# Optimization experiments

Measured on AMD Instinct MI355X. Metric: run time of the kernel, lower is better.

## Reference

```python
import jax, jax.numpy as jnp
import numpy as np

HEADS = 8
MAX_REL = 256
D_MODEL = 512
FFN_DIM = 2048
LN_EPS = 1e-3  # keras LayerNormalization default
NEG_INF = -1e9


def _layer_norm(x, gamma, beta):
    mu = jnp.mean(x, axis=-1, keepdims=True)
    var = jnp.var(x, axis=-1, keepdims=True)
    return (x - mu) * jax.lax.rsqrt(var + LN_EPS) * gamma + beta


def _mhra(q_in, k_in, v_in, mask, p):
    """Multi-head relative-position (Shaw-style) attention.
    mask: (B, Lq, Lk), 1.0 = masked position (added as -1e9).
    """
    B, Lq, D = q_in.shape
    Lk = k_in.shape[1]
    H = HEADS
    depth = D // H
    q = (q_in @ p['Wq'] + p['bq']).reshape(B, Lq, H, depth).transpose(0, 2, 1, 3)
    k = (k_in @ p['Wk'] + p['bk']).reshape(B, Lk, H, depth).transpose(0, 2, 1, 3)
    v = (v_in @ p['Wv'] + p['bv']).reshape(B, Lk, H, depth).transpose(0, 2, 1, 3)
    # content logits (B,H,Lq,Lk)
    logits = jnp.einsum('bhqd,bhkd->bhqk', q, k)
    # relative-position logits: project q onto clipped relative embeddings
    rel_q = jnp.einsum('bhqd,rd->bhqr', q, p['rel_emb'])  # (B,H,Lq,2K+1)
    rel_idx = jnp.clip(jnp.arange(Lk)[None, :] - jnp.arange(Lq)[:, None],
                       -MAX_REL, MAX_REL) + MAX_REL  # (Lq,Lk)
    rel_logits = jnp.take_along_axis(
        rel_q, jnp.broadcast_to(rel_idx[None, None], (B, H, Lq, Lk)), axis=-1)
    scores = (logits + rel_logits) / jnp.sqrt(jnp.asarray(depth, q.dtype))
    scores = scores + mask[:, None, :, :] * NEG_INF
    weights = jax.nn.softmax(scores, axis=-1)
    out = jnp.einsum('bhqk,bhkd->bhqd', weights, v)
    out = out.transpose(0, 2, 1, 3).reshape(B, Lq, D)
    out = out @ p['Wo'] + p['bo']
    return out, weights


def _make_attn_params(key, prefix):
    ks = jax.random.split(key, 5)
    s = 0.02
    return {
        prefix + 'Wq': jax.random.normal(ks[0], (D_MODEL, D_MODEL), jnp.float32) * s,
        prefix + 'bq': jnp.zeros((D_MODEL,), jnp.float32),
        prefix + 'Wk': jax.random.normal(ks[1], (D_MODEL, D_MODEL), jnp.float32) * s,
        prefix + 'bk': jnp.zeros((D_MODEL,), jnp.float32),
        prefix + 'Wv': jax.random.normal(ks[2], (D_MODEL, D_MODEL), jnp.float32) * s,
        prefix + 'bv': jnp.zeros((D_MODEL,), jnp.float32),
        prefix + 'Wo': jax.random.normal(ks[3], (D_MODEL, D_MODEL), jnp.float32) * s,
        prefix + 'bo': jnp.zeros((D_MODEL,), jnp.float32),
        prefix + 'rel_emb': jax.random.normal(ks[4], (2 * MAX_REL + 1, D_MODEL // HEADS), jnp.float32) * s,
        prefix + 'ln_g': jnp.ones((D_MODEL,), jnp.float32),
        prefix + 'ln_b': jnp.zeros((D_MODEL,), jnp.float32),
    }


def setup_inputs() -> dict:
    key = jax.random.key(0)
    ks = jax.random.split(key, 8)
    B, Lq, Lk = 8, 1024, 1024
    inputs = jax.random.normal(ks[0], (B, Lq, D_MODEL), jnp.float32)
    enc_kv = jax.random.normal(ks[1], (B, Lk, D_MODEL), jnp.float32)
    padding_mask = jnp.zeros((B, Lq, Lk), jnp.float32)  # no encoder padding
    causal = (jnp.arange(Lk)[None, :] > jnp.arange(Lq)[:, None]).astype(jnp.float32)
    lookahead_mask = jnp.broadcast_to(causal[None], (B, Lq, Lq)).astype(jnp.float32)
    d = {'inputs': inputs, 'enc_kv': enc_kv,
         'padding_mask': padding_mask, 'lookahead_mask': lookahead_mask,
         'training': 0}
    d.update(_make_attn_params(ks[2], 'sa_'))
    d.update(_make_attn_params(ks[3], 'ca_'))
    s = 0.02
    d['ffn_W1'] = jax.random.normal(ks[4], (D_MODEL, FFN_DIM), jnp.float32) * s
    d['ffn_b1'] = jnp.zeros((FFN_DIM,), jnp.float32)
    d['ffn_W2'] = jax.random.normal(ks[5], (FFN_DIM, D_MODEL), jnp.float32) * s
    d['ffn_b2'] = jnp.zeros((D_MODEL,), jnp.float32)
    d['ffn_ln_g'] = jnp.ones((D_MODEL,), jnp.float32)
    d['ffn_ln_b'] = jnp.zeros((D_MODEL,), jnp.float32)
    return d


def reference(inputs, enc_kv, padding_mask, lookahead_mask, training,
              sa_Wq, sa_bq, sa_Wk, sa_bk, sa_Wv, sa_bv, sa_Wo, sa_bo,
              sa_rel_emb, sa_ln_g, sa_ln_b,
              ca_Wq, ca_bq, ca_Wk, ca_bk, ca_Wv, ca_bv, ca_Wo, ca_bo,
              ca_rel_emb, ca_ln_g, ca_ln_b,
              ffn_W1, ffn_b1, ffn_W2, ffn_b2, ffn_ln_g, ffn_ln_b):
    sa = {'Wq': sa_Wq, 'bq': sa_bq, 'Wk': sa_Wk, 'bk': sa_bk,
          'Wv': sa_Wv, 'bv': sa_bv, 'Wo': sa_Wo, 'bo': sa_bo,
          'rel_emb': sa_rel_emb}
    ca = {'Wq': ca_Wq, 'bq': ca_bq, 'Wk': ca_Wk, 'bk': ca_bk,
          'Wv': ca_Wv, 'bv': ca_bv, 'Wo': ca_Wo, 'bo': ca_bo,
          'rel_emb': ca_rel_emb}
    # self attention + residual + norm (dropout identity at inference)
    attn_out, attn_w = _mhra(inputs, inputs, inputs, lookahead_mask, sa)
    attn_out = _layer_norm(inputs + attn_out, sa_ln_g, sa_ln_b)
    # cross attention + residual + norm
    ca_out, ca_w = _mhra(attn_out, enc_kv, enc_kv, padding_mask, ca)
    ca_out = _layer_norm(attn_out + ca_out, ca_ln_g, ca_ln_b)
    # pointwise FFN + residual + norm
    h = jax.nn.relu(ca_out @ ffn_W1 + ffn_b1) @ ffn_W2 + ffn_b2
    out = _layer_norm(h + ca_out, ffn_ln_g, ffn_ln_b)
    return out, attn_w, ca_w
```

## Files before the change

kernel.cpp:

```cpp
#include <hip/hip_runtime.h>
#include <hip/hip_bf16.h>
#include <cstdio>


typedef __attribute__((ext_vector_type(8))) short short8v;
typedef __attribute__((ext_vector_type(4))) short short4v;
typedef __attribute__((ext_vector_type(4))) float f32x4;

static __device__ __forceinline__ unsigned short f2bf(float f) {
    unsigned int u = __float_as_uint(f);
    unsigned int r = (u + 0x7fffu + ((u >> 16) & 1u)) >> 16;
    return (unsigned short)r;
}
static __device__ __forceinline__ float bf2f(unsigned short s) {
    return __uint_as_float(((unsigned int)s) << 16);
}

static __device__ __forceinline__ f32x4 mfma_bf16(short8v a, short8v b, f32x4 c) {
    return __builtin_amdgcn_mfma_f32_16x16x32_bf16(a, b, c, 0, 0, 0);
}

static __device__ __forceinline__ void async16(const void* g, void* l) {
    __builtin_amdgcn_global_load_lds(
        (const __attribute__((address_space(1))) unsigned int*)g,
        (__attribute__((address_space(3))) unsigned int*)l,
        16, 0, 0);
}

static __device__ __forceinline__ int swz8(int bid, int nwg) {
    return (bid & 7) * (nwg >> 3) + (bid >> 3);
}


static __device__ __forceinline__ void gemm_core(
    unsigned short* As, unsigned short* Bs,
    const unsigned short* __restrict__ A, int lda,
    const unsigned short* __restrict__ BT, int ldb,
    const float* __restrict__ bias, float* __restrict__ Cf,
    unsigned short* __restrict__ Cb, int ldc,
    int m0, int n0, int Kblk, int relu)
{
    const int t = threadIdx.x, lane = t & 63, w = t >> 6;
    const int wm = w >> 1, wn = w & 1;
    const int g = lane >> 4, l15 = lane & 15;
    f32x4 acc[4][4];
#pragma unroll
    for (int m = 0; m < 4; ++m)
#pragma unroll
        for (int n = 0; n < 4; ++n) acc[m][n] = (f32x4){0.f, 0.f, 0.f, 0.f};

    const int sgl8 = (lane & 7) ^ ((lane >> 3) & 7);
    for (int k0 = 0; k0 < Kblk; k0 += 64) {
#pragma unroll
        for (int i = 0; i < 4; ++i) {
            int rbase = w * 32 + i * 8;
            async16(A  + (size_t)(m0 + rbase + (lane >> 3)) * lda + k0 + sgl8 * 8,
                    As + rbase * 64);
            async16(BT + (size_t)(n0 + rbase + (lane >> 3)) * ldb + k0 + sgl8 * 8,
                    Bs + rbase * 64);
        }
        __syncthreads();
#pragma unroll
        for (int kk = 0; kk < 2; ++kk) {
            short8v a[4], b[4];
#pragma unroll
            for (int m = 0; m < 4; ++m) {
                int row = wm * 64 + m * 16 + l15;
                a[m] = *(const short8v*)&As[row * 64 + (((kk * 4 + g) ^ (row & 7))) * 8];
            }
#pragma unroll
            for (int n = 0; n < 4; ++n) {
                int row = wn * 64 + n * 16 + l15;
                b[n] = *(const short8v*)&Bs[row * 64 + (((kk * 4 + g) ^ (row & 7))) * 8];
            }
#pragma unroll
            for (int m = 0; m < 4; ++m)
#pragma unroll
                for (int n = 0; n < 4; ++n)
                    acc[m][n] = mfma_bf16(a[m], b[n], acc[m][n]);
        }
        __syncthreads();
    }
#pragma unroll
    for (int m = 0; m < 4; ++m) {
        int gm = m0 + wm * 64 + m * 16 + (lane >> 4) * 4;
#pragma unroll
        for (int n = 0; n < 4; ++n) {
            int gn = n0 + wn * 64 + n * 16 + (lane & 15);
            float bv = bias ? bias[gn] : 0.f;
#pragma unroll
            for (int j = 0; j < 4; ++j) {
                float v = acc[m][n][j] + bv;
                if (relu) v = fmaxf(v, 0.f);
                size_t off = (size_t)(gm + j) * ldc + gn;
                if (Cf) Cf[off] = v;
                if (Cb) Cb[off] = f2bf(v);
            }
        }
    }
}

__global__ __launch_bounds__(256) void gemm_std(
    const unsigned short* __restrict__ A, int lda,
    const unsigned short* __restrict__ BT, int ldb,
    const float* __restrict__ bias,
    float* __restrict__ Cf, unsigned short* __restrict__ Cb,
    int N, int Kblk, int relu)
{
    __shared__ __attribute__((aligned(16))) unsigned short As[128 * 64];
    __shared__ __attribute__((aligned(16))) unsigned short Bs[128 * 64];
    const int kz = blockIdx.z;
    const int nwg = gridDim.x * gridDim.y;
    const int s = swz8(blockIdx.x + gridDim.x * blockIdx.y, nwg);
    const int bx = s % gridDim.x, by = s / gridDim.x;
    const size_t part = (size_t)kz * gridDim.y * 128 * N;
    gemm_core(As, Bs, A + kz * Kblk, lda, BT + kz * Kblk, ldb,
              kz == 0 ? bias : nullptr,
              Cf ? Cf + part : nullptr, Cb, N,
              by * 128, bx * 128, Kblk, relu);
}

__global__ __launch_bounds__(256) void gemm_ca(
    const unsigned short* __restrict__ Ekv, const unsigned short* __restrict__ Xq,
    const unsigned short* __restrict__ WkvT, const unsigned short* __restrict__ WqT,
    const float* __restrict__ bkv, const float* __restrict__ bq,
    unsigned short* __restrict__ KV, unsigned short* __restrict__ Q)
{
    __shared__ __attribute__((aligned(16))) unsigned short As[128 * 64];
    __shared__ __attribute__((aligned(16))) unsigned short Bs[128 * 64];
    const int nwg = gridDim.x * gridDim.y;
    const int s = swz8(blockIdx.x + gridDim.x * blockIdx.y, nwg);
    const int bx = s % gridDim.x, by = s / gridDim.x;
    if (bx < 8)
        gemm_core(As, Bs, Ekv, 512, WkvT, 512, bkv, nullptr, KV, 1024,
                  by * 128, bx * 128, 512, 0);
    else
        gemm_core(As, Bs, Xq, 512, WqT, 512, bq, nullptr, Q, 512,
                  by * 128, (bx - 8) * 128, 512, 0);
}

__global__ __launch_bounds__(256, 3) void fused_attn(
    const unsigned short* __restrict__ Qp, int qstride,
    const unsigned short* __restrict__ Kp, int kstride,
    const unsigned short* __restrict__ Vt,
    const unsigned short* __restrict__ relW,
    const unsigned short* __restrict__ maskb,
    float* __restrict__ Wout,
    unsigned short* __restrict__ Hout)
{
    __shared__ __attribute__((aligned(16))) unsigned short Qs[16 * 64];
    __shared__ __attribute__((aligned(16))) unsigned short U[24576];
    __shared__ float Red[2][4][16];
    __shared__ unsigned short R512[16];
    unsigned short* Ks   = U;
    unsigned short* Pl   = U;
    unsigned short* RelV = U + 16384;
    unsigned short* Vs   = U + 16384;
    const int t = threadIdx.x, lane = t & 63, w = t >> 6;
    const int g = lane >> 4, l15 = lane & 15;
    const int s = swz8(blockIdx.x + gridDim.x * blockIdx.y, 4096);
    const int bh = s >> 6, b = bh >> 3, h = bh & 7;
    const int q0 = (s & 63) * 16;
    const int sgl8 = (lane & 7) ^ ((lane >> 3) & 7);

    if (w < 2) {
        int row = w * 8 + (lane >> 3);
        async16(Qp + (size_t)(b * 1024 + q0 + row) * qstride + h * 64 + sgl8 * 8,
                &Qs[w * 512]);
    }
    __syncthreads();

    short8v qa[2];
#pragma unroll
    for (int kk = 0; kk < 2; ++kk)
        qa[kk] = *(const short8v*)&Qs[l15 * 64 + (((kk * 4 + g) ^ (l15 & 7))) * 8];

    auto relTile = [&](int rs) {
        int rc = rs * 16 + l15;
        int re = rc > 512 ? 512 : rc;
        short8v b0 = *(const short8v*)(relW + (size_t)re * 64 + g * 8);
        short8v b1 = *(const short8v*)(relW + (size_t)re * 64 + 32 + g * 8);
        f32x4 r4 = (f32x4){0.f, 0.f, 0.f, 0.f};
        r4 = mfma_bf16(qa[0], b0, r4);
        r4 = mfma_bf16(qa[1], b1, r4);
        if (rs < 32) {
#pragma unroll
            for (int j = 0; j < 4; ++j)
                RelV[(g * 4 + j) * 512 + rs * 16 + l15] = f2bf(r4[j]);
        } else if (l15 == 0) {
#pragma unroll
            for (int j = 0; j < 4; ++j)
                R512[g * 4 + j] = f2bf(r4[j]);
        }
    };

    f32x4 acc[16];
#pragma unroll
    for (int i = 0; i < 16; ++i) acc[i] = (f32x4){0.f, 0.f, 0.f, 0.f};

#pragma unroll
    for (int qtr = 0; qtr < 4; ++qtr) {
#pragma unroll
        for (int c = 0; c < 8; ++c) {
            int rbase = w * 64 + c * 8;
            async16(Kp + (size_t)(b * 1024 + qtr * 256 + rbase + (lane >> 3)) * kstride
                       + h * 64 + sgl8 * 8,
                    &Ks[rbase * 64]);
        }
        relTile(8 * qtr + w);
        relTile(8 * qtr + w + 4);
        if (qtr == 3 && w == 0) relTile(32);
        __syncthreads();
#pragma unroll
        for (int n = 0; n < 4; ++n) {
            int row = w * 64 + n * 16 + l15;
            short8v kb0 = *(const short8v*)&Ks[row * 64 + ((g ^ (row & 7))) * 8];
            short8v kb1 = *(const short8v*)&Ks[row * 64 + (((4 + g) ^ (row & 7))) * 8];
            acc[qtr * 4 + n] = mfma_bf16(qa[0], kb0, acc[qtr * 4 + n]);
            acc[qtr * 4 + n] = mfma_bf16(qa[1], kb1, acc[qtr * 4 + n]);
        }
        __syncthreads();
    }

    const int qb = q0 + g * 4;
    const int ql = g * 4;
    const unsigned short* mrow = maskb + ((size_t)b * 1024 + qb) * 1024;
#pragma unroll
    for (int na = 0; na < 16; ++na) {
        int k = (na >> 2) * 256 + w * 64 + (na & 3) * 16 + l15;
#pragma unroll
        for (int j = 0; j < 4; ++j) {
            int q = qb + j;
            int d = k - q; d = d < -256 ? -256 : (d > 256 ? 256 : d);
            int idx = d + 256;
            float rel = (idx < 512) ? bf2f(RelV[(ql + j) * 512 + idx])
                                    : bf2f(R512[ql + j]);
            float mv = bf2f(mrow[(size_t)j * 1024 + k]);
            acc[na][j] = (acc[na][j] + rel) * 0.125f + mv;
        }
    }

    float mx[4];
#pragma unroll
    for (int j = 0; j < 4; ++j) {
        float m = acc[0][j];
#pragma unroll
        for (int na = 1; na < 16; ++na) m = fmaxf(m, acc[na][j]);
#pragma unroll
        for (int off = 1; off < 16; off <<= 1) m = fmaxf(m, __shfl_xor(m, off));
        mx[j] = m;
    }
    if (l15 == 0) {
#pragma unroll
        for (int j = 0; j < 4; ++j) Red[0][w][ql + j] = mx[j];
    }
    __syncthreads();
#pragma unroll
    for (int j = 0; j < 4; ++j) {
        float m = Red[0][0][ql + j];
        m = fmaxf(m, Red[0][1][ql + j]);
        m = fmaxf(m, Red[0][2][ql + j]);
        m = fmaxf(m, Red[0][3][ql + j]);
        mx[j] = m;
    }

    float sm[4] = {0.f, 0.f, 0.f, 0.f};
#pragma unroll
    for (int na = 0; na < 16; ++na)
#pragma unroll
        for (int j = 0; j < 4; ++j) {
            float e = __expf(acc[na][j] - mx[j]);
            acc[na][j] = e;
            sm[j] += e;
        }
#pragma unroll
    for (int j = 0; j < 4; ++j)
#pragma unroll
        for (int off = 1; off < 16; off <<= 1) sm[j] += __shfl_xor(sm[j], off);
    if (l15 == 0) {
#pragma unroll
        for (int j = 0; j < 4; ++j) Red[1][w][ql + j] = sm[j];
    }
    __syncthreads();
#pragma unroll
    for (int j = 0; j < 4; ++j) {
        float ssum = Red[1][0][ql + j] + Red[1][1][ql + j]
                   + Red[1][2][ql + j] + Red[1][3][ql + j];
        sm[j] = 1.0f / ssum;
    }

    float* wbase = Wout + ((size_t)bh * 1024 + qb) * 1024;
#pragma unroll
    for (int na = 0; na < 16; ++na) {
        int k = (na >> 2) * 256 + w * 64 + (na & 3) * 16 + l15;
#pragma unroll
        for (int j = 0; j < 4; ++j) {
            float p = acc[na][j] * sm[j];
            __builtin_nontemporal_store(p, &wbase[(size_t)j * 1024 + k]);
            Pl[((k >> 3) * 16 + (ql + j)) * 8 + (k & 7)] = f2bf(p);
        }
    }
    __syncthreads();

    f32x4 oacc = (f32x4){0.f, 0.f, 0.f, 0.f};
#pragma unroll
    for (int c = 0; c < 8; ++c) {
        {
            int idx = w * 4;
#pragma unroll
            for (int i = 0; i < 4; ++i) {
                int d = (idx + i) * 4 + (lane >> 4);
                int gl = (lane & 15) ^ (d & 15);
                async16(Vt + ((size_t)bh * 64 + d) * 1024 + c * 128 + gl * 8,
                        &Vs[(idx + i) * 512]);
            }
        }
        __syncthreads();
#pragma unroll
        for (int ks = 0; ks < 4; ++ks) {
            int kg = c * 4 + ks;
            short8v a = *(const short8v*)&Pl[((kg * 4 + g) * 16 + l15) * 8];
            int rowv = w * 16 + l15;
            short8v bb = *(const short8v*)&Vs[rowv * 128 + (((ks * 4 + g) ^ (rowv & 15))) * 8];
            oacc = mfma_bf16(a, bb, oacc);
        }
        __syncthreads();
    }
#pragma unroll
    for (int j = 0; j < 4; ++j)
        Hout[(size_t)(b * 1024 + q0 + g * 4 + j) * 512 + h * 64 + w * 16 + l15]
            = f2bf(oacc[j]);
}

__global__ __launch_bounds__(256) void transpose_v(
    const unsigned short* __restrict__ Vb, int stride, unsigned short* __restrict__ Vt)
{
    __shared__ unsigned short T[128][72];
    const int bh = blockIdx.y, b = bh >> 3, h = bh & 7;
    const int k0 = blockIdx.x * 128;
    const int t = threadIdx.x;
    {
        int r = t >> 1, half = t & 1;
        const unsigned short* gp = Vb + (size_t)(b * 1024 + k0 + r) * stride + h * 64 + half * 32;
#pragma unroll
        for (int i = 0; i < 8; ++i)
            *(short4v*)&T[r][half * 32 + i * 4] = *(const short4v*)(gp + i * 4);
    }
    __syncthreads();
    {
        int d = t >> 2, qtr = t & 3;
        unsigned short* gp = Vt + ((size_t)bh * 64 + d) * 1024 + k0 + qtr * 32;
#pragma unroll
        for (int i = 0; i < 32; i += 4) {
            short4v v;
            v.x = T[qtr * 32 + i + 0][d];
            v.y = T[qtr * 32 + i + 1][d];
            v.z = T[qtr * 32 + i + 2][d];
            v.w = T[qtr * 32 + i + 3][d];
            *(short4v*)(gp + i) = v;
        }
    }
}

__global__ __launch_bounds__(128) void ln512(
    const float* __restrict__ Xp0, const float* __restrict__ Xp1,
    const float* __restrict__ Res,
    const float* __restrict__ g, const float* __restrict__ be,
    float* __restrict__ out, unsigned short* __restrict__ outb)
{
    const size_t row = blockIdx.x;
    const int t = threadIdx.x;
    float4 x = *(const float4*)(Xp0 + row * 512 + t * 4);
    float4 r = *(const float4*)(Res + row * 512 + t * 4);
    x.x += r.x; x.y += r.y; x.z += r.z; x.w += r.w;
    if (Xp1) {
        float4 p = *(const float4*)(Xp1 + row * 512 + t * 4);
        x.x += p.x; x.y += p.y; x.z += p.z; x.w += p.w;
    }
    float s  = x.x + x.y + x.z + x.w;
    float ss = x.x * x.x + x.y * x.y + x.z * x.z + x.w * x.w;
#pragma unroll
    for (int o = 32; o > 0; o >>= 1) { s += __shfl_xor(s, o); ss += __shfl_xor(ss, o); }
    __shared__ float sm[2], sq[2];
    if ((t & 63) == 0) { sm[t >> 6] = s; sq[t >> 6] = ss; }
    __syncthreads();
    s = sm[0] + sm[1]; ss = sq[0] + sq[1];
    const float mean = s * (1.f / 512.f);
    const float var  = ss * (1.f / 512.f) - mean * mean;
    const float rstd = rsqrtf(var + 1e-3f);
    float4 gv = *(const float4*)(g + t * 4), bv = *(const float4*)(be + t * 4);
    float4 o;
    o.x = (x.x - mean) * rstd * gv.x + bv.x;
    o.y = (x.y - mean) * rstd * gv.y + bv.y;
    o.z = (x.z - mean) * rstd * gv.z + bv.z;
    o.w = (x.w - mean) * rstd * gv.w + bv.w;
    *(float4*)(out + row * 512 + t * 4) = o;
    if (outb) {
        short4v q4;
        q4.x = f2bf(o.x); q4.y = f2bf(o.y); q4.z = f2bf(o.z); q4.w = f2bf(o.w);
        *(short4v*)(outb + row * 512 + t * 4) = q4;
    }
}

static __device__ __forceinline__ void wt_tile(
    const float* __restrict__ W, unsigned short* __restrict__ WT,
    int K, int N, int k0, int n0)
{
    __shared__ float T[64][68];
    const int t = threadIdx.x;
    int r = t >> 4, c = (t & 15) * 4;
#pragma unroll
    for (int p = 0; p < 4; ++p) {
        float4 v = *(const float4*)(W + (size_t)(k0 + r + p * 16) * N + n0 + c);
        T[r + p * 16][c + 0] = v.x; T[r + p * 16][c + 1] = v.y;
        T[r + p * 16][c + 2] = v.z; T[r + p * 16][c + 3] = v.w;
    }
    __syncthreads();
#pragma unroll
    for (int p = 0; p < 4; ++p) {
        int n = r + p * 16;
        short4v o;
        o.x = f2bf(T[c + 0][n]); o.y = f2bf(T[c + 1][n]);
        o.z = f2bf(T[c + 2][n]); o.w = f2bf(T[c + 3][n]);
        *(short4v*)(WT + (size_t)(n0 + n) * K + k0 + c) = o;
    }
}

struct Ptr8 {
    const float* s[8];
    unsigned short* d[8];
};

__global__ __launch_bounds__(256) void wt_cast_all(
    Ptr8 p, const float* __restrict__ fW1, unsigned short* __restrict__ W1T,
    const float* __restrict__ fW2, unsigned short* __restrict__ W2T)
{
    const int bid = blockIdx.x;
    if (bid < 512) {
        int mat = bid >> 6, tile = bid & 63;
        wt_tile(p.s[mat], p.d[mat], 512, 512, (tile >> 3) * 64, (tile & 7) * 64);
    } else if (bid < 768) {
        int tile = bid - 512;
        wt_tile(fW1, W1T, 512, 2048, (tile >> 5) * 64, (tile & 31) * 64);
    } else {
        int tile = bid - 768;
        wt_tile(fW2, W2T, 2048, 512, (tile >> 3) * 64, (tile & 7) * 64);
    }
}

__global__ __launch_bounds__(256) void misc_prep(
    const float* __restrict__ sarel, const float* __restrict__ carel,
    unsigned short* __restrict__ relSA, unsigned short* __restrict__ relCA,
    const float* __restrict__ sabq, const float* __restrict__ sabk,
    const float* __restrict__ sabv, float* __restrict__ bqkv,
    const float* __restrict__ cabk, const float* __restrict__ cabv,
    float* __restrict__ bkv)
{
    const int bid = blockIdx.x, t = threadIdx.x;
    if (bid < 33) {
        int i = bid * 256 + t;
        if (i < 8208) {
            float4 v = *(const float4*)(sarel + (size_t)i * 4);
            short4v s;
            s.x = f2bf(v.x); s.y = f2bf(v.y); s.z = f2bf(v.z); s.w = f2bf(v.w);
            *(short4v*)(relSA + (size_t)i * 4) = s;
        }
    } else if (bid < 66) {
        int i = (bid - 33) * 256 + t;
        if (i < 8208) {
            float4 v = *(const float4*)(carel + (size_t)i * 4);
            short4v s;
            s.x = f2bf(v.x); s.y = f2bf(v.y); s.z = f2bf(v.z); s.w = f2bf(v.w);
            *(short4v*)(relCA + (size_t)i * 4) = s;
        }
    } else if (bid == 66) {
        for (int i = t; i < 1536; i += 256)
            bqkv[i] = i < 512 ? sabq[i] : (i < 1024 ? sabk[i - 512] : sabv[i - 1024]);
    } else {
        for (int i = t; i < 1024; i += 256)
            bkv[i] = i < 512 ? cabk[i] : cabv[i - 512];
    }
}

__global__ __launch_bounds__(256) void cast_all(
    const float* __restrict__ a, unsigned short* __restrict__ oa,
    const float* __restrict__ b, unsigned short* __restrict__ ob,
    const float* __restrict__ m0, unsigned short* __restrict__ om0,
    const float* __restrict__ m1, unsigned short* __restrict__ om1)
{
    size_t i = (size_t)blockIdx.x * 256 + threadIdx.x;
    const float* src; unsigned short* dst; float scale;
    if (i < 1048576)      { src = a;  dst = oa;  scale = 1.f; }
    else if (i < 2097152) { src = b;  dst = ob;  scale = 1.f; i -= 1048576; }
    else if (i < 4194304) { src = m0; dst = om0; scale = -1e9f; i -= 2097152; }
    else                  { src = m1; dst = om1; scale = -1e9f; i -= 4194304; }
    const float4* sp = (const float4*)(src + i * 4);
    float4 v;
    v.x = __builtin_nontemporal_load(&((const float*)sp)[0]);
    v.y = __builtin_nontemporal_load(&((const float*)sp)[1]);
    v.z = __builtin_nontemporal_load(&((const float*)sp)[2]);
    v.w = __builtin_nontemporal_load(&((const float*)sp)[3]);
    short4v s;
    s.x = f2bf(v.x * scale); s.y = f2bf(v.y * scale);
    s.z = f2bf(v.z * scale); s.w = f2bf(v.w * scale);
    *(short4v*)(dst + i * 4) = s;
}


extern "C" void kernel_launch(void* const* d_in, const int* in_sizes, int n_in,
                              void* d_out, int out_size, void* d_ws, size_t ws_size,
                              hipStream_t stream)
{
    (void)in_sizes; (void)n_in; (void)out_size;
    const float* inputs    = (const float*)d_in[0];
    const float* enc_kv    = (const float*)d_in[1];
    const float* pad_mask  = (const float*)d_in[2];
    const float* look_mask = (const float*)d_in[3];
    const float* saWq  = (const float*)d_in[5];
    const float* sabq  = (const float*)d_in[6];
    const float* saWk  = (const float*)d_in[7];
    const float* sabk  = (const float*)d_in[8];
    const float* saWv  = (const float*)d_in[9];
    const float* sabv  = (const float*)d_in[10];
    const float* saWo  = (const float*)d_in[11];
    const float* sabo  = (const float*)d_in[12];
    const float* sarel = (const float*)d_in[13];
    const float* salg  = (const float*)d_in[14];
    const float* salb  = (const float*)d_in[15];
    const float* caWq  = (const float*)d_in[16];
    const float* cabq  = (const float*)d_in[17];
    const float* caWk  = (const float*)d_in[18];
    const float* cabk  = (const float*)d_in[19];
    const float* caWv  = (const float*)d_in[20];
    const float* cabv  = (const float*)d_in[21];
    const float* caWo  = (const float*)d_in[22];
    const float* cabo  = (const float*)d_in[23];
    const float* carel = (const float*)d_in[24];
    const float* calg  = (const float*)d_in[25];
    const float* calb  = (const float*)d_in[26];
    const float* fW1   = (const float*)d_in[27];
    const float* fb1   = (const float*)d_in[28];
    const float* fW2   = (const float*)d_in[29];
    const float* fb2   = (const float*)d_in[30];
    const float* flg   = (const float*)d_in[31];
    const float* flb   = (const float*)d_in[32];

    float* out    = (float*)d_out;
    float* attn_w = out + (size_t)8 * 1024 * 512;
    float* ca_w   = attn_w + (size_t)8 * 8 * 1024 * 1024;

    char* ws = (char*)d_ws;
    size_t off = 0;
    unsigned short* WTa = (unsigned short*)(ws + off); off += 8519936;
    float* bqkv = (float*)(ws + off); off += 8192;
    float* bkv  = (float*)(ws + off); off += 8192;
    unsigned short* Abf   = (unsigned short*)(ws + off); off += 8388608;
    unsigned short* Ebf   = (unsigned short*)(ws + off); off += 8388608;
    unsigned short* x1bf  = (unsigned short*)(ws + off); off += 8388608;
    unsigned short* Qca   = (unsigned short*)(ws + off); off += 8388608;
    unsigned short* heads = (unsigned short*)(ws + off); off += 8388608;
    unsigned short* Vt    = (unsigned short*)(ws + off); off += 8388608;
    unsigned short* mskSA = (unsigned short*)(ws + off); off += 16777216;
    unsigned short* mskCA = (unsigned short*)(ws + off); off += 16777216;
    unsigned short* KV    = (unsigned short*)(ws + off); off += 16777216;
    unsigned short* big   = (unsigned short*)(ws + off); off += 33554432;
    float* x1 = (float*)(ws + off); off += 16777216;
    float* x2 = (float*)(ws + off); off += 16777216;
    float* Pb = (float*)(ws + off); off += 33554432;
    if (ws_size < off) {
        fprintf(stderr, "kernel_launch: ws too small (%zu < %zu)\n", ws_size, off);
        return;
    }
    float* Pb1 = Pb + 4194304;
    unsigned short* QKV    = big;
    unsigned short* hidden = big;
    unsigned short* x2bf   = Abf;

    unsigned short* saWqT = WTa + 0;
    unsigned short* saWkT = WTa + 262144;
    unsigned short* saWvT = WTa + 524288;
    unsigned short* saWoT = WTa + 786432;
    unsigned short* caWqT = WTa + 1048576;
    unsigned short* caWkT = WTa + 1310720;
    unsigned short* caWvT = WTa + 1572864;
    unsigned short* caWoT = WTa + 1835008;
    unsigned short* W1T   = WTa + 2097152;
    unsigned short* W2T   = WTa + 3145728;
    unsigned short* relSA = WTa + 4194304;
    unsigned short* relCA = WTa + 4227136;

    const dim3 T256(256), T128(128);

    Ptr8 p8;
    p8.s[0] = saWq; p8.d[0] = saWqT;
    p8.s[1] = saWk; p8.d[1] = saWkT;
    p8.s[2] = saWv; p8.d[2] = saWvT;
    p8.s[3] = saWo; p8.d[3] = saWoT;
    p8.s[4] = caWq; p8.d[4] = caWqT;
    p8.s[5] = caWk; p8.d[5] = caWkT;
    p8.s[6] = caWv; p8.d[6] = caWvT;
    p8.s[7] = caWo; p8.d[7] = caWoT;
    wt_cast_all<<<dim3(1024), T256, 0, stream>>>(p8, fW1, W1T, fW2, W2T);
    misc_prep<<<dim3(68), T256, 0, stream>>>(sarel, carel, relSA, relCA,
                                             sabq, sabk, sabv, bqkv, cabk, cabv, bkv);
    cast_all<<<dim3(24576), T256, 0, stream>>>(inputs, Abf, enc_kv, Ebf,
                                               look_mask, mskSA, pad_mask, mskCA);

    gemm_std<<<dim3(12, 64, 1), T256, 0, stream>>>(Abf, 512, WTa, 512, bqkv,
                                                   nullptr, QKV, 1536, 512, 0);
    transpose_v<<<dim3(8, 64), T256, 0, stream>>>(QKV + 1024, 1536, Vt);
    fused_attn<<<dim3(64, 64), T256, 0, stream>>>(QKV, 1536, QKV + 512, 1536, Vt,
                                                  relSA, mskSA, attn_w, heads);
    gemm_std<<<dim3(4, 64, 2), T256, 0, stream>>>(heads, 512, saWoT, 512, sabo,
                                                  Pb, nullptr, 512, 256, 0);
    ln512<<<dim3(8192), T128, 0, stream>>>(Pb, Pb1, inputs, salg, salb, x1, x1bf);

    gemm_ca<<<dim3(12, 64), T256, 0, stream>>>(Ebf, x1bf, caWkT, caWqT,
                                               bkv, cabq, KV, Qca);
    transpose_v<<<dim3(8, 64), T256, 0, stream>>>(KV + 512, 1024, Vt);
    fused_attn<<<dim3(64, 64), T256, 0, stream>>>(Qca, 512, KV, 1024, Vt,
                                                  relCA, mskCA, ca_w, heads);
    gemm_std<<<dim3(4, 64, 2), T256, 0, stream>>>(heads, 512, caWoT, 512, cabo,
                                                  Pb, nullptr, 512, 256, 0);
    ln512<<<dim3(8192), T128, 0, stream>>>(Pb, Pb1, x1, calg, calb, x2, x2bf);

    gemm_std<<<dim3(16, 64, 1), T256, 0, stream>>>(x2bf, 512, W1T, 512, fb1,
                                                   nullptr, hidden, 2048, 512, 1);
    gemm_std<<<dim3(4, 64, 2), T256, 0, stream>>>(hidden, 2048, W2T, 2048, fb2,
                                                  Pb, nullptr, 512, 1024, 0);
    ln512<<<dim3(8192), T128, 0, stream>>>(Pb, Pb1, x2, flg, flb, out, nullptr);
}
```

Baseline: 493.3 us.

## Skip fully masked key blocks in causal self-attention kernel

```diff
diff --git a/kernel.cpp b/kernel.cpp
--- a/kernel.cpp
+++ b/kernel.cpp
@@ -139,6 +139,7 @@
                   by * 128, (bx - 8) * 128, 512, 0);
 }
 
+template<int CAUSAL>
 __global__ __launch_bounds__(256, 3) void fused_attn(
     const unsigned short* __restrict__ Qp, int qstride,
     const unsigned short* __restrict__ Kp, int kstride,
@@ -151,11 +152,10 @@
     __shared__ __attribute__((aligned(16))) unsigned short Qs[16 * 64];
     __shared__ __attribute__((aligned(16))) unsigned short U[24576];
     __shared__ float Red[2][4][16];
-    __shared__ unsigned short R512[16];
-    unsigned short* Ks   = U;
-    unsigned short* Pl   = U;
-    unsigned short* RelV = U + 16384;
-    unsigned short* Vs   = U + 16384;
+    unsigned short* Ks  = U;
+    unsigned short* Rel = U;
+    unsigned short* Pl  = U;
+    unsigned short* Vs  = U + 16384;
     const int t = threadIdx.x, lane = t & 63, w = t >> 6;
     const int g = lane >> 4, l15 = lane & 15;
     const int s = swz8(blockIdx.x + gridDim.x * blockIdx.y, 4096);
@@ -163,6 +163,10 @@
     const int q0 = (s & 63) * 16;
     const int sgl8 = (lane & 7) ^ ((lane >> 3) & 7);
 
+    const int nq   = CAUSAL ? (q0 >> 8) + 1 : 4;
+    const int nact = CAUSAL ? nq * 4 : 16;
+    const int nc   = CAUSAL ? (q0 >> 7) + 1 : 8;
+
     if (w < 2) {
         int row = w * 8 + (lane >> 3);
         async16(Qp + (size_t)(b * 1024 + q0 + row) * qstride + h * 64 + sgl8 * 8,
@@ -175,7 +179,32 @@
     for (int kk = 0; kk < 2; ++kk)
         qa[kk] = *(const short8v*)&Qs[l15 * 64 + (((kk * 4 + g) ^ (l15 & 7))) * 8];
 
-    auto relTile = [&](int rs) {
+    f32x4 acc[16];
+#pragma unroll
+    for (int i = 0; i < 16; ++i) acc[i] = (f32x4){0.f, 0.f, 0.f, 0.f};
+
+    for (int qtr = 0; qtr < nq; ++qtr) {
+#pragma unroll
+        for (int c = 0; c < 8; ++c) {
+            int rbase = w * 64 + c * 8;
+            async16(Kp + (size_t)(b * 1024 + qtr * 256 + rbase + (lane >> 3)) * kstride
+                       + h * 64 + sgl8 * 8,
+                    &Ks[rbase * 64]);
+        }
+        __syncthreads();
+#pragma unroll
+        for (int n = 0; n < 4; ++n) {
+            int row = w * 64 + n * 16 + l15;
+            short8v kb0 = *(const short8v*)&Ks[row * 64 + ((g ^ (row & 7))) * 8];
+            short8v kb1 = *(const short8v*)&Ks[row * 64 + (((4 + g) ^ (row & 7))) * 8];
+            acc[qtr * 4 + n] = mfma_bf16(qa[0], kb0, acc[qtr * 4 + n]);
+            acc[qtr * 4 + n] = mfma_bf16(qa[1], kb1, acc[qtr * 4 + n]);
+        }
+        __syncthreads();
+    }
+
+    const int nrs = CAUSAL ? 17 : 33;
+    for (int rs = w; rs < nrs; rs += 4) {
         int rc = rs * 16 + l15;
         int re = rc > 512 ? 512 : rc;
         short8v b0 = *(const short8v*)(relW + (size_t)re * 64 + g * 8);
@@ -183,58 +212,24 @@
         f32x4 r4 = (f32x4){0.f, 0.f, 0.f, 0.f};
         r4 = mfma_bf16(qa[0], b0, r4);
         r4 = mfma_bf16(qa[1], b1, r4);
-        if (rs < 32) {
-#pragma unroll
-            for (int j = 0; j < 4; ++j)
-                RelV[(g * 4 + j) * 512 + rs * 16 + l15] = f2bf(r4[j]);
-        } else if (l15 == 0) {
-#pragma unroll
-            for (int j = 0; j < 4; ++j)
-                R512[g * 4 + j] = f2bf(r4[j]);
-        }
-    };
-
-    f32x4 acc[16];
-#pragma unroll
-    for (int i = 0; i < 16; ++i) acc[i] = (f32x4){0.f, 0.f, 0.f, 0.f};
-
-#pragma unroll
-    for (int qtr = 0; qtr < 4; ++qtr) {
-#pragma unroll
-        for (int c = 0; c < 8; ++c) {
-            int rbase = w * 64 + c * 8;
-            async16(Kp + (size_t)(b * 1024 + qtr * 256 + rbase + (lane >> 3)) * kstride
-                       + h * 64 + sgl8 * 8,
-                    &Ks[rbase * 64]);
-        }
-        relTile(8 * qtr + w);
-        relTile(8 * qtr + w + 4);
-        if (qtr == 3 && w == 0) relTile(32);
-        __syncthreads();
-#pragma unroll
-        for (int n = 0; n < 4; ++n) {
-            int row = w * 64 + n * 16 + l15;
-            short8v kb0 = *(const short8v*)&Ks[row * 64 + ((g ^ (row & 7))) * 8];
-            short8v kb1 = *(const short8v*)&Ks[row * 64 + (((4 + g) ^ (row & 7))) * 8];
-            acc[qtr * 4 + n] = mfma_bf16(qa[0], kb0, acc[qtr * 4 + n]);
-            acc[qtr * 4 + n] = mfma_bf16(qa[1], kb1, acc[qtr * 4 + n]);
-        }
-        __syncthreads();
-    }
+#pragma unroll
+        for (int j = 0; j < 4; ++j)
+            Rel[(g * 4 + j) * 528 + rs * 16 + l15] = f2bf(r4[j]);
+    }
+    __syncthreads();
 
     const int qb = q0 + g * 4;
     const int ql = g * 4;
     const unsigned short* mrow = maskb + ((size_t)b * 1024 + qb) * 1024;
 #pragma unroll
     for (int na = 0; na < 16; ++na) {
+        if (na >= nact) break;
         int k = (na >> 2) * 256 + w * 64 + (na & 3) * 16 + l15;
 #pragma unroll
         for (int j = 0; j < 4; ++j) {
             int q = qb + j;
             int d = k - q; d = d < -256 ? -256 : (d > 256 ? 256 : d);
-            int idx = d + 256;
-            float rel = (idx < 512) ? bf2f(RelV[(ql + j) * 512 + idx])
-                                    : bf2f(R512[ql + j]);
+            float rel = bf2f(Rel[(ql + j) * 528 + d + 256]);
             float mv = bf2f(mrow[(size_t)j * 1024 + k]);
             acc[na][j] = (acc[na][j] + rel) * 0.125f + mv;
         }
@@ -245,7 +240,10 @@
     for (int j = 0; j < 4; ++j) {
         float m = acc[0][j];
 #pragma unroll
-        for (int na = 1; na < 16; ++na) m = fmaxf(m, acc[na][j]);
+        for (int na = 1; na < 16; ++na) {
+            if (na >= nact) break;
+            m = fmaxf(m, acc[na][j]);
+        }
 #pragma unroll
         for (int off = 1; off < 16; off <<= 1) m = fmaxf(m, __shfl_xor(m, off));
         mx[j] = m;
@@ -266,13 +264,15 @@
 
     float sm[4] = {0.f, 0.f, 0.f, 0.f};
 #pragma unroll
-    for (int na = 0; na < 16; ++na)
+    for (int na = 0; na < 16; ++na) {
+        if (na >= nact) break;
 #pragma unroll
         for (int j = 0; j < 4; ++j) {
             float e = __expf(acc[na][j] - mx[j]);
             acc[na][j] = e;
             sm[j] += e;
         }
+    }
 #pragma unroll
     for (int j = 0; j < 4; ++j)
 #pragma unroll
@@ -293,18 +293,23 @@
 #pragma unroll
     for (int na = 0; na < 16; ++na) {
         int k = (na >> 2) * 256 + w * 64 + (na & 3) * 16 + l15;
-#pragma unroll
-        for (int j = 0; j < 4; ++j) {
-            float p = acc[na][j] * sm[j];
-            __builtin_nontemporal_store(p, &wbase[(size_t)j * 1024 + k]);
-            Pl[((k >> 3) * 16 + (ql + j)) * 8 + (k & 7)] = f2bf(p);
+        if (na < nact) {
+#pragma unroll
+            for (int j = 0; j < 4; ++j) {
+                float p = acc[na][j] * sm[j];
+                __builtin_nontemporal_store(p, &wbase[(size_t)j * 1024 + k]);
+                Pl[((k >> 3) * 16 + (ql + j)) * 8 + (k & 7)] = f2bf(p);
+            }
+        } else {
+#pragma unroll
+            for (int j = 0; j < 4; ++j)
+                __builtin_nontemporal_store(0.0f, &wbase[(size_t)j * 1024 + k]);
         }
     }
     __syncthreads();
 
     f32x4 oacc = (f32x4){0.f, 0.f, 0.f, 0.f};
-#pragma unroll
-    for (int c = 0; c < 8; ++c) {
+    for (int c = 0; c < nc; ++c) {
         {
             int idx = w * 4;
 #pragma unroll
@@ -609,8 +614,8 @@
     gemm_std<<<dim3(12, 64, 1), T256, 0, stream>>>(Abf, 512, WTa, 512, bqkv,
                                                    nullptr, QKV, 1536, 512, 0);
     transpose_v<<<dim3(8, 64), T256, 0, stream>>>(QKV + 1024, 1536, Vt);
-    fused_attn<<<dim3(64, 64), T256, 0, stream>>>(QKV, 1536, QKV + 512, 1536, Vt,
-                                                  relSA, mskSA, attn_w, heads);
+    fused_attn<1><<<dim3(64, 64), T256, 0, stream>>>(QKV, 1536, QKV + 512, 1536, Vt,
+                                                     relSA, mskSA, attn_w, heads);
     gemm_std<<<dim3(4, 64, 2), T256, 0, stream>>>(heads, 512, saWoT, 512, sabo,
                                                   Pb, nullptr, 512, 256, 0);
     ln512<<<dim3(8192), T128, 0, stream>>>(Pb, Pb1, inputs, salg, salb, x1, x1bf);
@@ -618,8 +623,8 @@
     gemm_ca<<<dim3(12, 64), T256, 0, stream>>>(Ebf, x1bf, caWkT, caWqT,
                                                bkv, cabq, KV, Qca);
     transpose_v<<<dim3(8, 64), T256, 0, stream>>>(KV + 512, 1024, Vt);
-    fused_attn<<<dim3(64, 64), T256, 0, stream>>>(Qca, 512, KV, 1024, Vt,
-                                                  relCA, mskCA, ca_w, heads);
+    fused_attn<0><<<dim3(64, 64), T256, 0, stream>>>(Qca, 512, KV, 1024, Vt,
+                                                     relCA, mskCA, ca_w, heads);
     gemm_std<<<dim3(4, 64, 2), T256, 0, stream>>>(heads, 512, caWoT, 512, cabo,
                                                   Pb, nullptr, 512, 256, 0);
     ln512<<<dim3(8192), T128, 0, stream>>>(Pb, Pb1, x1, calg, calb, x2, x2bf);
```

After: 687.8 us. +39.4%, slower.
